# Kernel optimization log

Measured on AMD Instinct MI355X. Metric: run time of the kernel, lower is better.

## Reference

```python
import jax, jax.numpy as jnp
import numpy as np

VOCAB, H, MAXLEN = 50257, 1024, 128


def setup_inputs() -> dict:
    key = jax.random.key(0)
    ks = jax.random.split(key, 14)
    s = 0.02  # init scale
    f32 = jnp.float32
    return {
        "x": jax.random.randint(ks[0], (1,), 0, VOCAB),
        "h": jax.random.normal(ks[1], (1, 1, H), f32),
        "encoder_outputs": jax.random.normal(ks[2], (MAXLEN, H), f32),
        "emb": jax.random.normal(ks[3], (VOCAB, H), f32) * s,
        "W_attn": jax.random.normal(ks[4], (MAXLEN, 2 * H), f32) * s,
        "b_attn": jnp.zeros((MAXLEN,), f32),
        "W_comb": jax.random.normal(ks[5], (H, 2 * H), f32) * s,
        "b_comb": jnp.zeros((H,), f32),
        "w_ih": jax.random.normal(ks[6], (3 * H, H), f32) * s,
        "w_hh": jax.random.normal(ks[7], (3 * H, H), f32) * s,
        "b_ih": jnp.zeros((3 * H,), f32),
        "b_hh": jnp.zeros((3 * H,), f32),
        "W_out": jax.random.normal(ks[8], (VOCAB, H), f32) * s,
        "b_out": jnp.zeros((VOCAB,), f32),
    }


def reference(x, h, encoder_outputs, emb, W_attn, b_attn, W_comb, b_comb,
              w_ih, w_hh, b_ih, b_hh, W_out, b_out):
    # Single decode step (batch=1, seq=1); dropout in eval mode (identity).
    e = emb[x]                       # [1, H] embedded token
    h0 = h[0]                        # [1, H] hidden state
    # attention over encoder outputs
    attn_w = jax.nn.softmax(jnp.concatenate([e, h0], axis=1) @ W_attn.T + b_attn, axis=1)  # [1, MAXLEN]
    attn_applied = attn_w @ encoder_outputs                                                 # [1, H]
    # combine + relu
    g = jax.nn.relu(jnp.concatenate([e, attn_applied], axis=1) @ W_comb.T + b_comb)        # [1, H]
    # single-step GRU (PyTorch gate order: r, z, n)
    gi = g @ w_ih.T + b_ih           # [1, 3H]
    gh = h0 @ w_hh.T + b_hh          # [1, 3H]
    i_r, i_z, i_n = jnp.split(gi, 3, axis=1)
    h_r, h_z, h_n = jnp.split(gh, 3, axis=1)
    r = jax.nn.sigmoid(i_r + h_r)
    z = jax.nn.sigmoid(i_z + h_z)
    n = jnp.tanh(i_n + r * h_n)
    h_new = (1.0 - z) * n + z * h0   # [1, H]
    out = jax.nn.log_softmax(h_new @ W_out.T + b_out, axis=1)  # [1, VOCAB]
    return out, h_new[None], attn_w
```

## Files before the change

### kernel.cpp

```cpp
#include <hip/hip_runtime.h>
#include <hip/hip_bf16.h>
#include <math.h>

#define H 1024
#define MAXLEN 128
#define VOCAB 50257
#define NB_OUT ((VOCAB + 3) / 4)

__device__ inline float wave_reduce_sum(float v) {
    #pragma unroll
    for (int off = 32; off > 0; off >>= 1) v += __shfl_down(v, off);
    return v;
}

__global__ void k_attn_logits(const int* x, const float* h, const float* emb,
                              const float* W_attn, const float* b_attn, float* logits) {
    const int row = blockIdx.x;
    const float4* w4 = (const float4*)(W_attn + row * (2 * H));
    const float4* e4 = (const float4*)(emb + (long long)x[0] * H);
    const float4* h4 = (const float4*)h;
    float acc = 0.f;
    int t = threadIdx.x;
    #pragma unroll
    for (int i = 0; i < 2; i++) {
        int idx = t + i * 256;
        float4 wv = w4[idx];
        float4 cv = (idx < 256) ? e4[idx] : h4[idx - 256];
        acc += wv.x * cv.x + wv.y * cv.y + wv.z * cv.z + wv.w * cv.w;
    }
    __shared__ float red[4];
    int lane = t & 63, wid = t >> 6;
    acc = wave_reduce_sum(acc);
    if (lane == 0) red[wid] = acc;
    __syncthreads();
    if (t == 0)
        logits[row] = red[0] + red[1] + red[2] + red[3] + b_attn[row];
}

__global__ void k_attn_sm_apply(const float* logits, const float* enc,
                                float* attn_applied, float* out_attn) {
    __shared__ float buf[MAXLEN];
    __shared__ float w[MAXLEN];
    int t = threadIdx.x;
    if (t < MAXLEN) buf[t] = logits[t];
    __syncthreads();
    float m = -INFINITY;
    #pragma unroll 8
    for (int k = 0; k < MAXLEN; k++) m = fmaxf(m, buf[k]);
    if (t < MAXLEN) w[t] = expf(buf[t] - m);
    __syncthreads();
    float s = 0.f;
    #pragma unroll 8
    for (int k = 0; k < MAXLEN; k++) s += w[k];
    float inv = 1.f / s;
    int j = blockIdx.x * blockDim.x + t;
    float acc = 0.f;
    #pragma unroll 8
    for (int k = 0; k < MAXLEN; k++) acc += w[k] * enc[k * H + j];
    attn_applied[j] = acc * inv;
    if (blockIdx.x == 0 && t < MAXLEN) out_attn[t] = w[t] * inv;
}

__global__ void k_combine(const int* x, const float* emb, const float* attn_applied,
                          const float* W_comb, const float* b_comb, float* g) {
    int wid = threadIdx.x >> 6, lane = threadIdx.x & 63;
    int row = blockIdx.x * 4 + wid;
    const float4* w4 = (const float4*)(W_comb + (long long)row * (2 * H));
    const float4* e4 = (const float4*)(emb + (long long)x[0] * H);
    const float4* a4 = (const float4*)attn_applied;
    float acc = 0.f;
    #pragma unroll
    for (int i = 0; i < 8; i++) {
        int idx = lane + i * 64;
        float4 wv = w4[idx];
        float4 cv = (idx < 256) ? e4[idx] : a4[idx - 256];
        acc += wv.x * cv.x + wv.y * cv.y + wv.z * cv.z + wv.w * cv.w;
    }
    acc = wave_reduce_sum(acc);
    if (lane == 0) g[row] = fmaxf(acc + b_comb[row], 0.f);
}

__global__ void k_gru_mm(const float* g, const float* h,
                         const float* w_ih, const float* w_hh,
                         const float* b_ih, const float* b_hh,
                         float* gi, float* gh) {
    int wid = threadIdx.x >> 6, lane = threadIdx.x & 63;
    int gRow = blockIdx.x * 4 + wid;
    const float* vec;
    const float* mat;
    const float* bias;
    float* out;
    int row;
    if (gRow < 3 * H) { row = gRow; vec = g; mat = w_ih; bias = b_ih; out = gi; }
    else { row = gRow - 3 * H; vec = h; mat = w_hh; bias = b_hh; out = gh; }
    const float4* w4 = (const float4*)(mat + (long long)row * H);
    const float4* v4 = (const float4*)vec;
    float acc = 0.f;
    #pragma unroll
    for (int i = 0; i < 4; i++) {
        int idx = lane + i * 64;
        float4 wv = w4[idx];
        float4 vv = v4[idx];
        acc += wv.x * vv.x + wv.y * vv.y + wv.z * vv.z + wv.w * vv.w;
    }
    acc = wave_reduce_sum(acc);
    if (lane == 0) out[row] = acc + bias[row];
}

__global__ void k_gates(const float* gi, const float* gh, const float* h, float* h_new) {
    int j = threadIdx.x;
    float r = 1.f / (1.f + expf(-(gi[j] + gh[j])));
    float z = 1.f / (1.f + expf(-(gi[j + H] + gh[j + H])));
    float n = tanhf(gi[j + 2 * H] + r * gh[j + 2 * H]);
    h_new[j] = (1.f - z) * n + z * h[j];
}

__global__ void k_out_matvec(const float* hn, const float* W_out, const float* b_out,
                             float* out, float* pmax, float* psum) {
    int wid = threadIdx.x >> 6, lane = threadIdx.x & 63;
    int row = blockIdx.x * 4 + wid;
    __shared__ float lm[4];
    float logit = -INFINITY;
    if (row < VOCAB) {
        const float4* w4 = (const float4*)(W_out + (long long)row * H);
        const float4* h4 = (const float4*)hn;
        float acc = 0.f;
        #pragma unroll
        for (int i = 0; i < 4; i++) {
            int idx = lane + i * 64;
            float4 wv = w4[idx];
            float4 hv = h4[idx];
            acc += wv.x * hv.x + wv.y * hv.y + wv.z * hv.z + wv.w * hv.w;
        }
        acc = wave_reduce_sum(acc);
        if (lane == 0) { logit = acc + b_out[row]; out[row] = logit; }
    }
    if (lane == 0) lm[wid] = logit;
    __syncthreads();
    if (threadIdx.x == 0) {
        float m = fmaxf(fmaxf(lm[0], lm[1]), fmaxf(lm[2], lm[3]));
        float s = 0.f;
        #pragma unroll
        for (int i = 0; i < 4; i++)
            if (lm[i] != -INFINITY) s += expf(lm[i] - m);
        pmax[blockIdx.x] = m;
        psum[blockIdx.x] = s;
    }
}

__global__ void k_lse_merge(const float* pmax, const float* psum, float* c) {
    __shared__ float red[16];
    __shared__ float Msh;
    int lane = threadIdx.x & 63, wid = threadIdx.x >> 6;
    float m = -INFINITY;
    for (int i = threadIdx.x; i < NB_OUT; i += blockDim.x) m = fmaxf(m, pmax[i]);
    #pragma unroll
    for (int off = 32; off > 0; off >>= 1) m = fmaxf(m, __shfl_down(m, off));
    if (lane == 0) red[wid] = m;
    __syncthreads();
    if (threadIdx.x == 0) {
        float mm = red[0];
        for (int i = 1; i < 16; i++) mm = fmaxf(mm, red[i]);
        Msh = mm;
    }
    __syncthreads();
    float M = Msh;
    float s = 0.f;
    for (int i = threadIdx.x; i < NB_OUT; i += blockDim.x) s += psum[i] * expf(pmax[i] - M);
    s = wave_reduce_sum(s);
    if (lane == 0) red[wid] = s;
    __syncthreads();
    if (threadIdx.x == 0) {
        float ss = 0.f;
        for (int i = 0; i < 16; i++) ss += red[i];
        c[0] = M + logf(ss);
    }
}

__global__ void k_sub(float* out, const float* c) {
    int v = blockIdx.x * blockDim.x + threadIdx.x;
    if (v < VOCAB) out[v] -= c[0];
}

extern "C" void kernel_launch(void* const* d_in, const int* in_sizes, int n_in,
                              void* d_out, int out_size, void* d_ws, size_t ws_size,
                              hipStream_t stream) {
    const int*   x     = (const int*)d_in[0];
    const float* h     = (const float*)d_in[1];
    const float* enc   = (const float*)d_in[2];
    const float* emb   = (const float*)d_in[3];
    const float* W_attn= (const float*)d_in[4];
    const float* b_attn= (const float*)d_in[5];
    const float* W_comb= (const float*)d_in[6];
    const float* b_comb= (const float*)d_in[7];
    const float* w_ih  = (const float*)d_in[8];
    const float* w_hh  = (const float*)d_in[9];
    const float* b_ih  = (const float*)d_in[10];
    const float* b_hh  = (const float*)d_in[11];
    const float* W_out = (const float*)d_in[12];
    const float* b_out = (const float*)d_in[13];

    float* out      = (float*)d_out;
    float* out_h    = out + VOCAB;
    float* out_attn = out + VOCAB + H;

    float* ws       = (float*)d_ws;
    float* logits128   = ws;
    float* attn_applied= ws + 256;
    float* g           = ws + 1280;
    float* gi          = ws + 2304;
    float* gh          = ws + 5376;
    float* lse_c       = ws + 8448;
    float* pmax        = ws + 9216;
    float* psum        = ws + 22272;

    k_attn_logits<<<MAXLEN, 256, 0, stream>>>(x, h, emb, W_attn, b_attn, logits128);
    k_attn_sm_apply<<<H / 256, 256, 0, stream>>>(logits128, enc, attn_applied, out_attn);
    k_combine<<<H / 4, 256, 0, stream>>>(x, emb, attn_applied, W_comb, b_comb, g);
    k_gru_mm<<<(6 * H) / 4, 256, 0, stream>>>(g, h, w_ih, w_hh, b_ih, b_hh, gi, gh);
    k_gates<<<1, H, 0, stream>>>(gi, gh, h, out_h);
    k_out_matvec<<<NB_OUT, 256, 0, stream>>>(out_h, W_out, b_out, out, pmax, psum);
    k_lse_merge<<<1, 1024, 0, stream>>>(pmax, psum, lse_c);
    k_sub<<<(VOCAB + 255) / 256, 256, 0, stream>>>(out, lse_c);
}
```

Measured before the change: 74.12 us.

## Fuse GRU matvecs with gates, batch output rows per wave, regrid attention kernels

Merges the GRU input/hidden matvecs and the gate nonlinearity into one kernel with a block per hidden unit, which removes a launch and the gi/gh round trip through global memory. The output projection now computes two vocab rows per wave and keeps the hidden vector in registers, halving the number of partial max/sum entries. Attention logits use one wave per row, and the attention-apply kernel runs on eight blocks of 128 active threads instead of four blocks of 256. The final subtract uses 1024-thread blocks. These changes trade lower launch count and traffic for different occupancy and per-wave load patterns.

```diff
diff --git a/kernel.cpp b/kernel.cpp
--- a/kernel.cpp
+++ b/kernel.cpp
@@ -1,11 +1,12 @@
 #include <hip/hip_runtime.h>
-#include <hip/hip_bf16.h>
 #include <math.h>
 
 #define H 1024
 #define MAXLEN 128
 #define VOCAB 50257
-#define NB_OUT ((VOCAB + 3) / 4)
+
+#define ROWS_PB 8
+#define NB_OUT ((VOCAB + ROWS_PB - 1) / ROWS_PB)
 
 __device__ inline float wave_reduce_sum(float v) {
     #pragma unroll
@@ -13,52 +14,53 @@
     return v;
 }
 
+__device__ inline float dot4(float4 a, float4 b) {
+    return a.x * b.x + a.y * b.y + a.z * b.z + a.w * b.w;
+}
+
 __global__ void k_attn_logits(const int* x, const float* h, const float* emb,
                               const float* W_attn, const float* b_attn, float* logits) {
-    const int row = blockIdx.x;
+    const int lane = threadIdx.x & 63, wid = threadIdx.x >> 6;
+    const int row = blockIdx.x * 4 + wid;
     const float4* w4 = (const float4*)(W_attn + row * (2 * H));
     const float4* e4 = (const float4*)(emb + (long long)x[0] * H);
     const float4* h4 = (const float4*)h;
     float acc = 0.f;
-    int t = threadIdx.x;
-    #pragma unroll
-    for (int i = 0; i < 2; i++) {
-        int idx = t + i * 256;
+    #pragma unroll
+    for (int i = 0; i < 8; i++) {
+        int idx = lane + i * 64;
         float4 wv = w4[idx];
         float4 cv = (idx < 256) ? e4[idx] : h4[idx - 256];
-        acc += wv.x * cv.x + wv.y * cv.y + wv.z * cv.z + wv.w * cv.w;
-    }
-    __shared__ float red[4];
-    int lane = t & 63, wid = t >> 6;
+        acc += dot4(wv, cv);
+    }
     acc = wave_reduce_sum(acc);
-    if (lane == 0) red[wid] = acc;
-    __syncthreads();
-    if (t == 0)
-        logits[row] = red[0] + red[1] + red[2] + red[3] + b_attn[row];
+    if (lane == 0) logits[row] = acc + b_attn[row];
 }
 
 __global__ void k_attn_sm_apply(const float* logits, const float* enc,
                                 float* attn_applied, float* out_attn) {
     __shared__ float buf[MAXLEN];
-    __shared__ float w[MAXLEN];
+    __shared__ float wsm[MAXLEN];
     int t = threadIdx.x;
     if (t < MAXLEN) buf[t] = logits[t];
     __syncthreads();
     float m = -INFINITY;
     #pragma unroll 8
     for (int k = 0; k < MAXLEN; k++) m = fmaxf(m, buf[k]);
-    if (t < MAXLEN) w[t] = expf(buf[t] - m);
+    if (t < MAXLEN) wsm[t] = expf(buf[t] - m);
     __syncthreads();
     float s = 0.f;
     #pragma unroll 8
-    for (int k = 0; k < MAXLEN; k++) s += w[k];
+    for (int k = 0; k < MAXLEN; k++) s += wsm[k];
     float inv = 1.f / s;
-    int j = blockIdx.x * blockDim.x + t;
-    float acc = 0.f;
-    #pragma unroll 8
-    for (int k = 0; k < MAXLEN; k++) acc += w[k] * enc[k * H + j];
-    attn_applied[j] = acc * inv;
-    if (blockIdx.x == 0 && t < MAXLEN) out_attn[t] = w[t] * inv;
+    if (t < MAXLEN) {
+        int j = blockIdx.x * MAXLEN + t;
+        float acc = 0.f;
+        #pragma unroll 8
+        for (int k = 0; k < MAXLEN; k++) acc += wsm[k] * enc[k * H + j];
+        attn_applied[j] = acc * inv;
+        if (blockIdx.x == 0) out_attn[t] = wsm[t] * inv;
+    }
 }
 
 __global__ void k_combine(const int* x, const float* emb, const float* attn_applied,
@@ -74,74 +76,111 @@
         int idx = lane + i * 64;
         float4 wv = w4[idx];
         float4 cv = (idx < 256) ? e4[idx] : a4[idx - 256];
-        acc += wv.x * cv.x + wv.y * cv.y + wv.z * cv.z + wv.w * cv.w;
+        acc += dot4(wv, cv);
     }
     acc = wave_reduce_sum(acc);
     if (lane == 0) g[row] = fmaxf(acc + b_comb[row], 0.f);
 }
 
-__global__ void k_gru_mm(const float* g, const float* h,
-                         const float* w_ih, const float* w_hh,
-                         const float* b_ih, const float* b_hh,
-                         float* gi, float* gh) {
-    int wid = threadIdx.x >> 6, lane = threadIdx.x & 63;
-    int gRow = blockIdx.x * 4 + wid;
-    const float* vec;
-    const float* mat;
-    const float* bias;
-    float* out;
-    int row;
-    if (gRow < 3 * H) { row = gRow; vec = g; mat = w_ih; bias = b_ih; out = gi; }
-    else { row = gRow - 3 * H; vec = h; mat = w_hh; bias = b_hh; out = gh; }
-    const float4* w4 = (const float4*)(mat + (long long)row * H);
-    const float4* v4 = (const float4*)vec;
-    float acc = 0.f;
-    #pragma unroll
-    for (int i = 0; i < 4; i++) {
-        int idx = lane + i * 64;
-        float4 wv = w4[idx];
-        float4 vv = v4[idx];
-        acc += wv.x * vv.x + wv.y * vv.y + wv.z * vv.z + wv.w * vv.w;
-    }
-    acc = wave_reduce_sum(acc);
-    if (lane == 0) out[row] = acc + bias[row];
-}
-
-__global__ void k_gates(const float* gi, const float* gh, const float* h, float* h_new) {
-    int j = threadIdx.x;
-    float r = 1.f / (1.f + expf(-(gi[j] + gh[j])));
-    float z = 1.f / (1.f + expf(-(gi[j + H] + gh[j + H])));
-    float n = tanhf(gi[j + 2 * H] + r * gh[j + 2 * H]);
-    h_new[j] = (1.f - z) * n + z * h[j];
+__global__ void k_gru_fused(const float* g, const float* h,
+                            const float* w_ih, const float* w_hh,
+                            const float* b_ih, const float* b_hh, float* h_new) {
+    const int j = blockIdx.x, t = threadIdx.x;
+    const int lane = t & 63, wid = t >> 6;
+    __shared__ float red6[4][6];
+    const float4* g4 = (const float4*)g;
+    const float4* h4 = (const float4*)h;
+    float4 vg = g4[t];
+    float4 vh = h4[t];
+    float a6[6];
+    #pragma unroll
+    for (int gt = 0; gt < 3; gt++) {
+        const float4* wi = (const float4*)(w_ih + (long long)(j + gt * H) * H);
+        const float4* wh = (const float4*)(w_hh + (long long)(j + gt * H) * H);
+        a6[gt]     = dot4(wi[t], vg);
+        a6[3 + gt] = dot4(wh[t], vh);
+    }
+    #pragma unroll
+    for (int k = 0; k < 6; k++) {
+        float v = a6[k];
+        #pragma unroll
+        for (int off = 32; off > 0; off >>= 1) v += __shfl_down(v, off);
+        if (lane == 0) red6[wid][k] = v;
+    }
+    __syncthreads();
+    if (t == 0) {
+        float d[6];
+        #pragma unroll
+        for (int k = 0; k < 6; k++)
+            d[k] = red6[0][k] + red6[1][k] + red6[2][k] + red6[3][k];
+        float gi_r = d[0] + b_ih[j];
+        float gi_z = d[1] + b_ih[j + H];
+        float gi_n = d[2] + b_ih[j + 2 * H];
+        float gh_r = d[3] + b_hh[j];
+        float gh_z = d[4] + b_hh[j + H];
+        float gh_n = d[5] + b_hh[j + 2 * H];
+        float r = 1.f / (1.f + expf(-(gi_r + gh_r)));
+        float z = 1.f / (1.f + expf(-(gi_z + gh_z)));
+        float n = tanhf(gi_n + r * gh_n);
+        h_new[j] = (1.f - z) * n + z * h[j];
+    }
 }
 
 __global__ void k_out_matvec(const float* hn, const float* W_out, const float* b_out,
                              float* out, float* pmax, float* psum) {
-    int wid = threadIdx.x >> 6, lane = threadIdx.x & 63;
-    int row = blockIdx.x * 4 + wid;
-    __shared__ float lm[4];
-    float logit = -INFINITY;
-    if (row < VOCAB) {
-        const float4* w4 = (const float4*)(W_out + (long long)row * H);
-        const float4* h4 = (const float4*)hn;
-        float acc = 0.f;
-        #pragma unroll
-        for (int i = 0; i < 4; i++) {
-            int idx = lane + i * 64;
-            float4 wv = w4[idx];
-            float4 hv = h4[idx];
-            acc += wv.x * hv.x + wv.y * hv.y + wv.z * hv.z + wv.w * hv.w;
+    const int t = threadIdx.x;
+    const int lane = t & 63, wid = t >> 6;
+    const int row0 = blockIdx.x * ROWS_PB + wid * 2;
+    __shared__ float lm[ROWS_PB];
+
+    const float4* h4 = (const float4*)hn;
+    float4 hreg[4];
+    #pragma unroll
+    for (int i = 0; i < 4; i++) hreg[i] = h4[lane + i * 64];
+
+    float l0 = -INFINITY, l1 = -INFINITY;
+    if (row0 + 1 < VOCAB) {
+        const float4* w0 = (const float4*)(W_out + (long long)row0 * H);
+        const float4* w1 = (const float4*)(W_out + (long long)(row0 + 1) * H);
+        float4 a0[4], a1[4];
+        #pragma unroll
+        for (int i = 0; i < 4; i++) a0[i] = w0[lane + i * 64];
+        #pragma unroll
+        for (int i = 0; i < 4; i++) a1[i] = w1[lane + i * 64];
+        float acc0 = 0.f, acc1 = 0.f;
+        #pragma unroll
+        for (int i = 0; i < 4; i++) { acc0 += dot4(a0[i], hreg[i]); acc1 += dot4(a1[i], hreg[i]); }
+        acc0 = wave_reduce_sum(acc0);
+        acc1 = wave_reduce_sum(acc1);
+        if (lane == 0) {
+            l0 = acc0 + b_out[row0];
+            l1 = acc1 + b_out[row0 + 1];
+            out[row0] = l0;
+            out[row0 + 1] = l1;
         }
-        acc = wave_reduce_sum(acc);
-        if (lane == 0) { logit = acc + b_out[row]; out[row] = logit; }
-    }
-    if (lane == 0) lm[wid] = logit;
-    __syncthreads();
-    if (threadIdx.x == 0) {
-        float m = fmaxf(fmaxf(lm[0], lm[1]), fmaxf(lm[2], lm[3]));
+    } else {
+        for (int r = row0; r < VOCAB && r < row0 + 2; r++) {
+            const float4* w4 = (const float4*)(W_out + (long long)r * H);
+            float acc = 0.f;
+            #pragma unroll
+            for (int i = 0; i < 4; i++) acc += dot4(w4[lane + i * 64], hreg[i]);
+            acc = wave_reduce_sum(acc);
+            if (lane == 0) {
+                float lv = acc + b_out[r];
+                out[r] = lv;
+                if (r == row0) l0 = lv; else l1 = lv;
+            }
+        }
+    }
+    if (lane == 0) { lm[wid * 2] = l0; lm[wid * 2 + 1] = l1; }
+    __syncthreads();
+    if (t == 0) {
+        float m = -INFINITY;
+        #pragma unroll
+        for (int i = 0; i < ROWS_PB; i++) m = fmaxf(m, lm[i]);
         float s = 0.f;
         #pragma unroll
-        for (int i = 0; i < 4; i++)
+        for (int i = 0; i < ROWS_PB; i++)
             if (lm[i] != -INFINITY) s += expf(lm[i] - m);
         pmax[blockIdx.x] = m;
         psum[blockIdx.x] = s;
@@ -204,22 +243,19 @@
     float* out_h    = out + VOCAB;
     float* out_attn = out + VOCAB + H;
 
-    float* ws       = (float*)d_ws;
+    float* ws          = (float*)d_ws;
     float* logits128   = ws;
     float* attn_applied= ws + 256;
-    float* g           = ws + 1280;
-    float* gi          = ws + 2304;
-    float* gh          = ws + 5376;
-    float* lse_c       = ws + 8448;
-    float* pmax        = ws + 9216;
-    float* psum        = ws + 22272;
-
-    k_attn_logits<<<MAXLEN, 256, 0, stream>>>(x, h, emb, W_attn, b_attn, logits128);
-    k_attn_sm_apply<<<H / 256, 256, 0, stream>>>(logits128, enc, attn_applied, out_attn);
-    k_combine<<<H / 4, 256, 0, stream>>>(x, emb, attn_applied, W_comb, b_comb, g);
-    k_gru_mm<<<(6 * H) / 4, 256, 0, stream>>>(g, h, w_ih, w_hh, b_ih, b_hh, gi, gh);
-    k_gates<<<1, H, 0, stream>>>(gi, gh, h, out_h);
+    float* g_vec       = ws + 1280;
+    float* lse_c       = ws + 2304;
+    float* pmax        = ws + 4096;
+    float* psum        = ws + 12288;
+
+    k_attn_logits<<<MAXLEN / 4, 256, 0, stream>>>(x, h, emb, W_attn, b_attn, logits128);
+    k_attn_sm_apply<<<H / MAXLEN, 256, 0, stream>>>(logits128, enc, attn_applied, out_attn);
+    k_combine<<<H / 4, 256, 0, stream>>>(x, emb, attn_applied, W_comb, b_comb, g_vec);
+    k_gru_fused<<<H, 256, 0, stream>>>(g_vec, h, w_ih, w_hh, b_ih, b_hh, out_h);
     k_out_matvec<<<NB_OUT, 256, 0, stream>>>(out_h, W_out, b_out, out, pmax, psum);
     k_lse_merge<<<1, 1024, 0, stream>>>(pmax, psum, lse_c);
-    k_sub<<<(VOCAB + 255) / 256, 256, 0, stream>>>(out, lse_c);
-}
+    k_sub<<<(VOCAB + 1023) / 1024, 1024, 0, stream>>>(out, lse_c);
+}
```

Result: faster. 71.31 us (-3.8%).
